# Kernel optimization log

Measured on AMD Instinct MI355X. Metric: run time of the kernel, lower is better.

## Reference

```python
import jax, jax.numpy as jnp
import numpy as np

B, C, H, W = 4, 256, 48, 48
HEADS, DH = 8, 64
HID = HEADS * DH
EPS = 1e-5
SCALE = DH ** -0.5


def setup_inputs() -> dict:
    key = jax.random.key(0)
    ks = jax.random.split(key, 8)
    return {
        "tensor": jax.random.normal(ks[0], (B, C, H, W), jnp.float32),
        "norm_g": jnp.ones((C,), jnp.float32),                      # ChanLayerNorm gamma
        "w_qkv": jax.random.normal(ks[1], (3 * HID, C), jnp.float32) * 0.02,  # 1x1 conv, no bias
        "dw_q": jax.random.normal(ks[2], (HID, 1, 3, 3), jnp.float32) * 0.1,  # depthwise 3x3
        "dw_k": jax.random.normal(ks[3], (HID, 1, 3, 3), jnp.float32) * 0.1,
        "dw_v": jax.random.normal(ks[4], (HID, 1, 3, 3), jnp.float32) * 0.1,
        "w_out": jax.random.normal(ks[5], (C, HID), jnp.float32) * 0.02,      # 1x1 conv out
        "b_out": jnp.zeros((C,), jnp.float32),
    }


def _rope(t):
    # t: (b, h, s, d) -- rotary embedding over flattened spatial positions
    s, d = t.shape[-2], t.shape[-1]
    inv_freq = 1.0 / (10000.0 ** (jnp.arange(0, d, 2, dtype=jnp.float32) / d))
    freqs = jnp.arange(s, dtype=jnp.float32)[:, None] * inv_freq[None, :]     # (s, d/2)
    emb = jnp.concatenate([freqs, freqs], axis=-1)                            # (s, d)
    cos, sin = jnp.cos(emb), jnp.sin(emb)
    t1, t2 = t[..., : d // 2], t[..., d // 2 :]
    rot = jnp.concatenate([-t2, t1], axis=-1)
    return t * cos + rot * sin


def _dwconv(x, w):
    # depthwise 3x3, padding=1 (Primer conv), groups = channels
    return jax.lax.conv_general_dilated(
        x, w, window_strides=(1, 1), padding="SAME",
        feature_group_count=x.shape[1],
        dimension_numbers=("NCHW", "OIHW", "NCHW"))


def reference(tensor, norm_g, w_qkv, dw_q, dw_k, dw_v, w_out, b_out):
    x = tensor
    # ChanLayerNorm: normalize over channel dim
    mean = jnp.mean(x, axis=1, keepdims=True)
    var = jnp.var(x, axis=1, keepdims=True)
    xn = (x - mean) * jax.lax.rsqrt(var + EPS) * norm_g[None, :, None, None]
    # 1x1 conv to qkv
    qkv = jnp.einsum("bchw,oc->bohw", xn, w_qkv)
    q, k, v = jnp.split(qkv, 3, axis=1)
    q, k, v = _dwconv(q, dw_q), _dwconv(k, dw_k), _dwconv(v, dw_v)
    # b (h d) x y -> b h (x y) d
    def to_seq(t):
        b = t.shape[0]
        return t.reshape(b, HEADS, DH, H * W).transpose(0, 1, 3, 2)
    q, k, v = to_seq(q), to_seq(k), to_seq(v)
    q, k = _rope(q), _rope(k)
    q = q * SCALE
    sim = jnp.einsum("bhid,bhjd->bhij", q, k)
    attn = jax.nn.softmax(sim, axis=-1)
    out = jnp.einsum("bhij,bhjd->bhid", attn, v)
    # b h (x y) d -> b (h d) x y
    out = out.transpose(0, 1, 3, 2).reshape(out.shape[0], HID, H, W)
    return jnp.einsum("bchw,oc->bohw", out, w_out) + b_out[None, :, None, None]
```

## Files before the change

### kernel.cpp

```cpp
#include <hip/hip_runtime.h>
#include <math.h>

#define SS 2304
#define C_IN 256
#define HID 512
#define QKV3 1536
#define HEADS 8
#define DH 64
#define BATCH 4
#define EPSV 1e-5f
#define SCALEV 0.125f

typedef short s8v __attribute__((ext_vector_type(8)));
typedef float f4v __attribute__((ext_vector_type(4)));
typedef unsigned int u4v __attribute__((ext_vector_type(4)));
typedef unsigned int uint32;

static __device__ inline unsigned short f2bf(float x) {
    unsigned int u = __float_as_uint(x);
    u += 0x7fffu + ((u >> 16) & 1u);
    return (unsigned short)(u >> 16);
}
static __device__ inline float bf2f(unsigned short h) {
    return __uint_as_float((unsigned int)h << 16);
}
static __device__ inline f4v mm(s8v a, s8v b, f4v c) {
    return __builtin_amdgcn_mfma_f32_16x16x32_bf16(a, b, c, 0, 0, 0);
}
static __device__ inline s8v pk4(uint32 a, uint32 b, uint32 c, uint32 d) {
    u4v t; t[0] = a; t[1] = b; t[2] = c; t[3] = d;
    return __builtin_bit_cast(s8v, t);
}
static __device__ inline uint32 pkhl(float p) {
    unsigned int u = __float_as_uint(p);
    unsigned int uh = u + (0x7fffu + ((u >> 16) & 1u));
    unsigned short h = (unsigned short)(uh >> 16);
    float r = p - __uint_as_float((unsigned int)h << 16);
    unsigned short l = (unsigned short)(__float_as_uint(r) >> 16);
    return (uint32)h | ((uint32)l << 16);
}
static __device__ inline uint32 rot16(uint32 u) { return (u >> 16) | (u << 16); }

__global__ void prep_wg(const float* __restrict__ w, const float* __restrict__ g,
                        float* __restrict__ wg, float* __restrict__ wsum) {
    __shared__ float red[256];
    int o = blockIdx.x, c = threadIdx.x;
    float v = w[o * C_IN + c] * g[c];
    wg[o * C_IN + c] = v;
    red[c] = v;
    __syncthreads();
    for (int st = 128; st > 0; st >>= 1) {
        if (c < st) red[c] += red[c + st];
        __syncthreads();
    }
    if (c == 0) wsum[o] = red[0];
}

__global__ void prep_rope(float* __restrict__ cosT, float* __restrict__ sinT) {
    int idx = blockIdx.x * 256 + threadIdx.x;
    if (idx >= SS * 32) return;
    int s = idx >> 5, f = idx & 31;
    double inv = pow(10000.0, -(double)f / 32.0);
    double ang = (double)s * inv;
    cosT[idx] = (float)cos(ang);
    sinT[idx] = (float)sin(ang);
}

__global__ void prep_stats(const float* __restrict__ x, float* __restrict__ mean,
                           float* __restrict__ rstd) {
    int p = blockIdx.x * 256 + threadIdx.x;
    int b = p / SS, s = p % SS;
    const float* xp = x + (size_t)b * C_IN * SS + s;
    float sm = 0.f;
    for (int c = 0; c < C_IN; ++c) sm += xp[(size_t)c * SS];
    float mu = sm * (1.0f / C_IN);
    float vs = 0.f;
    for (int c = 0; c < C_IN; ++c) { float d = xp[(size_t)c * SS] - mu; vs += d * d; }
    mean[p] = mu;
    rstd[p] = rsqrtf(vs * (1.0f / C_IN) + EPSV);
}

__global__ __launch_bounds__(256) void qkv_gemm(
    const float* __restrict__ x, const float* __restrict__ wg,
    const float* __restrict__ wsum, const float* __restrict__ mean,
    const float* __restrict__ rstd, float* __restrict__ qkv) {
    __shared__ float As[16][132];
    __shared__ float Bs[16][132];
    int b = blockIdx.z;
    int m0 = blockIdx.y * 128;
    int n0 = blockIdx.x * 128;
    int t = threadIdx.x;
    int tx = t & 15, ty = t >> 4;
    float acc[8][8] = {};
    const float* xb = x + (size_t)b * C_IN * SS;
    for (int k0 = 0; k0 < C_IN; k0 += 16) {
#pragma unroll
        for (int i = 0; i < 8; ++i) {
            int idx = t + i * 256;
            int kk = idx & 15, row = idx >> 4;
            As[kk][row] = wg[(m0 + row) * C_IN + k0 + kk];
            int ssi = idx & 127, cc = idx >> 7;
            Bs[cc][ssi] = xb[(size_t)(k0 + cc) * SS + n0 + ssi];
        }
        __syncthreads();
#pragma unroll
        for (int kk = 0; kk < 16; ++kk) {
            float4 a0 = *(const float4*)&As[kk][ty * 8];
            float4 a1 = *(const float4*)&As[kk][ty * 8 + 4];
            float4 b0 = *(const float4*)&Bs[kk][tx * 8];
            float4 b1 = *(const float4*)&Bs[kk][tx * 8 + 4];
            float am[8] = {a0.x, a0.y, a0.z, a0.w, a1.x, a1.y, a1.z, a1.w};
            float bn[8] = {b0.x, b0.y, b0.z, b0.w, b1.x, b1.y, b1.z, b1.w};
#pragma unroll
            for (int r = 0; r < 8; ++r)
#pragma unroll
                for (int c = 0; c < 8; ++c) acc[r][c] += am[r] * bn[c];
        }
        __syncthreads();
    }
    float mnv[8], rsv[8];
#pragma unroll
    for (int c = 0; c < 8; ++c) {
        int n = n0 + tx * 8 + c;
        mnv[c] = mean[b * SS + n];
        rsv[c] = rstd[b * SS + n];
    }
#pragma unroll
    for (int r = 0; r < 8; ++r) {
        int m = m0 + ty * 8 + r;
        float ws = wsum[m];
        float* dst = qkv + ((size_t)b * QKV3 + m) * SS + n0 + tx * 8;
        float ov[8];
#pragma unroll
        for (int c = 0; c < 8; ++c) ov[c] = rsv[c] * (acc[r][c] - mnv[c] * ws);
        *(float4*)dst = make_float4(ov[0], ov[1], ov[2], ov[3]);
        *(float4*)(dst + 4) = make_float4(ov[4], ov[5], ov[6], ov[7]);
    }
}

__global__ __launch_bounds__(256) void conv_rope(
    const float* __restrict__ qkv, const float* __restrict__ dwq,
    const float* __restrict__ dwk, const float* __restrict__ dwv,
    const float* __restrict__ cosT, const float* __restrict__ sinT,
    unsigned short* __restrict__ qhi, unsigned short* __restrict__ qlo,
    unsigned short* __restrict__ khi, unsigned short* __restrict__ klo,
    uint32* __restrict__ vtint) {
    __shared__ float tile[64][65];
    int b = blockIdx.z;
    int part = blockIdx.y >> 3;
    int h = blockIdx.y & 7;
    int s0 = blockIdx.x * 64;
    int t = threadIdx.x;
    int sl = t & 63, dgrp = t >> 6;
    int s = s0 + sl;
    int y = s / 48, xx = s - y * 48;
    int bh = b * HEADS + h;
    const float* dw = (part == 0) ? dwq : (part == 1) ? dwk : dwv;
#pragma unroll
    for (int i = 0; i < 16; ++i) {
        int d = dgrp * 16 + i;
        int cch = part * HID + h * DH + d;
        const float* src = qkv + ((size_t)b * QKV3 + cch) * SS;
        const float* wp = dw + (h * DH + d) * 9;
        float acc = 0.f;
#pragma unroll
        for (int dy = -1; dy <= 1; ++dy) {
            int yy = y + dy;
            if (yy < 0 || yy >= 48) continue;
#pragma unroll
            for (int dx = -1; dx <= 1; ++dx) {
                int xv = xx + dx;
                if (xv < 0 || xv >= 48) continue;
                acc += wp[(dy + 1) * 3 + (dx + 1)] * src[yy * 48 + xv];
            }
        }
        if (part == 2) {
            size_t o = ((size_t)bh * DH + d) * SS + s;
            unsigned short hu = f2bf(acc);
            unsigned short lu = (unsigned short)(__float_as_uint(acc - bf2f(hu)) >> 16);
            vtint[o] = (uint32)hu | ((uint32)lu << 16);
        } else {
            tile[d][sl] = acc;
        }
    }
    if (part == 2) return;
    __syncthreads();
    int d2 = t & 63, srow = t >> 6;
    unsigned short* hiA = (part == 0) ? qhi : khi;
    unsigned short* loA = (part == 0) ? qlo : klo;
#pragma unroll
    for (int i = 0; i < 16; ++i) {
        int sp = srow + 4 * i;
        float v0 = tile[d2][sp];
        float vp = tile[d2 ^ 32][sp];
        int f = d2 & 31;
        float cv = cosT[(s0 + sp) * 32 + f];
        float sv = sinT[(s0 + sp) * 32 + f];
        float rot = (d2 < 32) ? -vp : vp;
        float val = v0 * cv + rot * sv;
        if (part == 0) val *= SCALEV;
        size_t o = ((size_t)bh * SS + s0 + sp) * DH + d2;
        unsigned short hu = f2bf(val);
        hiA[o] = hu;
        loA[o] = f2bf(val - bf2f(hu));
    }
}

__global__ __launch_bounds__(256, 2) void attn_mfma(
    const unsigned short* __restrict__ qhi, const unsigned short* __restrict__ qlo,
    const unsigned short* __restrict__ khi, const unsigned short* __restrict__ klo,
    const uint32* __restrict__ vtint,
    float* __restrict__ Opart, float* __restrict__ lpart) {
    __shared__ float lds[4][64][68];
    __shared__ float lsl[4][64];
    int bh = blockIdx.z;
    int jh = blockIdx.y;
    int i0 = blockIdx.x * 64;
    int t = threadIdx.x;
    int wv = t >> 6;
    int lane = t & 63;
    int l15 = lane & 15;
    int quad = lane >> 4;

    s8v qf[4][4];
#pragma unroll
    for (int ig = 0; ig < 4; ++ig) {
        size_t qb = ((size_t)bh * SS + i0 + ig * 16 + l15) * DH + quad * 8;
        qf[ig][0] = *(const s8v*)(qhi + qb);
        qf[ig][1] = *(const s8v*)(qhi + qb + 32);
        qf[ig][2] = *(const s8v*)(qlo + qb);
        qf[ig][3] = *(const s8v*)(qlo + qb + 32);
    }
    f4v oacc[4][4];
#pragma unroll
    for (int dt = 0; dt < 4; ++dt)
#pragma unroll
        for (int ig = 0; ig < 4; ++ig) oacc[dt][ig] = (f4v){0.f, 0.f, 0.f, 0.f};
    float lsum[4] = {0.f, 0.f, 0.f, 0.f};

    const size_t kbh = (size_t)bh * SS * DH;
    const uint32* vbase = vtint + (size_t)bh * DH * SS;
    const int jbase = jh * 1152 + wv * 16;

    s8v kc[2][4], vc[2][4];
    auto ldK = [&](int s, s8v* K) {
        size_t row = kbh + (size_t)(jbase + s * 64 + l15) * DH + quad * 8;
        K[0] = *(const s8v*)(khi + row);
        K[1] = *(const s8v*)(khi + row + 32);
        K[2] = *(const s8v*)(klo + row);
        K[3] = *(const s8v*)(klo + row + 32);
    };
    auto ldV = [&](int s, s8v* V) {
        size_t col = (size_t)(jbase + s * 64 + quad * 4);
#pragma unroll
        for (int dt = 0; dt < 4; ++dt)
            V[dt] = __builtin_bit_cast(
                s8v, *(const u4v*)(vbase + (size_t)(dt * 16 + l15) * SS + col));
    };
    ldK(0, kc[0]);
    ldV(0, vc[0]);
#pragma unroll 2
    for (int s = 0; s < 18; ++s) {
        int cur = s & 1, nxt = cur ^ 1;
        if (s + 1 < 18) { ldK(s + 1, kc[nxt]); ldV(s + 1, vc[nxt]); }
        f4v sv[4];
#pragma unroll
        for (int ig = 0; ig < 4; ++ig) {
            f4v sx = {0.f, 0.f, 0.f, 0.f};
            sx = mm(kc[cur][0], qf[ig][0], sx);
            sx = mm(kc[cur][1], qf[ig][1], sx);
            sx = mm(kc[cur][0], qf[ig][2], sx);
            sx = mm(kc[cur][1], qf[ig][3], sx);
            sx = mm(kc[cur][2], qf[ig][0], sx);
            sx = mm(kc[cur][3], qf[ig][1], sx);
            sv[ig] = sx;
        }
        s8v B1[4], B2[4];
#pragma unroll
        for (int ig = 0; ig < 4; ++ig) {
            float p0 = __expf(sv[ig][0]), p1 = __expf(sv[ig][1]);
            float p2 = __expf(sv[ig][2]), p3 = __expf(sv[ig][3]);
            lsum[ig] += (p0 + p1) + (p2 + p3);
            uint32 u0 = pkhl(p0), u1 = pkhl(p1), u2 = pkhl(p2), u3 = pkhl(p3);
            B1[ig] = pk4(u0, u1, u2, u3);
            B2[ig] = pk4(rot16(u0), rot16(u1), rot16(u2), rot16(u3));
        }
#pragma unroll
        for (int dt = 0; dt < 4; ++dt)
#pragma unroll
            for (int ig = 0; ig < 4; ++ig) {
                oacc[dt][ig] = mm(vc[cur][dt], B1[ig], oacc[dt][ig]);
                oacc[dt][ig] = mm(vc[cur][dt], B2[ig], oacc[dt][ig]);
            }
    }
#pragma unroll
    for (int ig = 0; ig < 4; ++ig) {
        float v = lsum[ig];
        v += __shfl_xor(v, 16);
        v += __shfl_xor(v, 32);
        if (quad == 0) lsl[wv][ig * 16 + l15] = v;
    }
#pragma unroll
    for (int dt = 0; dt < 4; ++dt)
#pragma unroll
        for (int ig = 0; ig < 4; ++ig)
#pragma unroll
            for (int r = 0; r < 4; ++r)
                lds[wv][dt * 16 + quad * 4 + r][ig * 16 + l15] = oacc[dt][ig][r];
    __syncthreads();
    int d = t >> 2, qg = (t & 3) * 16;
    size_t ob = (((size_t)jh * 32 + bh) * DH + d) * SS + i0 + qg;
#pragma unroll
    for (int j4 = 0; j4 < 4; ++j4) {
        float4 a0 = *(const float4*)&lds[0][d][qg + j4 * 4];
        float4 a1 = *(const float4*)&lds[1][d][qg + j4 * 4];
        float4 a2 = *(const float4*)&lds[2][d][qg + j4 * 4];
        float4 a3 = *(const float4*)&lds[3][d][qg + j4 * 4];
        float4 rr;
        rr.x = (a0.x + a1.x) + (a2.x + a3.x);
        rr.y = (a0.y + a1.y) + (a2.y + a3.y);
        rr.z = (a0.z + a1.z) + (a2.z + a3.z);
        rr.w = (a0.w + a1.w) + (a2.w + a3.w);
        *(float4*)(Opart + ob + j4 * 4) = rr;
    }
    if (t < 64) {
        float v = (lsl[0][t] + lsl[1][t]) + (lsl[2][t] + lsl[3][t]);
        lpart[((size_t)jh * 32 + bh) * SS + i0 + t] = v;
    }
}

__global__ __launch_bounds__(256) void combine(
    const float* __restrict__ Opart, const float* __restrict__ lpart,
    float* __restrict__ OT) {
    int g = blockIdx.x * 256 + threadIdx.x;
    int s4 = g % (SS / 4);
    int rest = g / (SS / 4);
    int bh = rest >> 6;
    size_t base = (size_t)rest * SS + s4 * 4;
    float4 o0 = *(const float4*)(Opart + base);
    float4 o1 = *(const float4*)(Opart + base + (size_t)32 * DH * SS);
    float4 l0 = *(const float4*)(lpart + (size_t)bh * SS + s4 * 4);
    float4 l1 = *(const float4*)(lpart + (size_t)(32 + bh) * SS + s4 * 4);
    float4 r;
    r.x = (o0.x + o1.x) / (l0.x + l1.x);
    r.y = (o0.y + o1.y) / (l0.y + l1.y);
    r.z = (o0.z + o1.z) / (l0.z + l1.z);
    r.w = (o0.w + o1.w) / (l0.w + l1.w);
    *(float4*)(OT + base) = r;
}

__global__ __launch_bounds__(256) void outproj(
    const float* __restrict__ OT, const float* __restrict__ w_out,
    const float* __restrict__ b_out, float* __restrict__ out) {
    __shared__ float As[16][68];
    __shared__ float Bs[16][132];
    int b = blockIdx.z;
    int m0 = blockIdx.y * 64;
    int n0 = blockIdx.x * 128;
    int t = threadIdx.x;
    int tx = t & 15, ty = t >> 4;
    float acc[4][8] = {};
    for (int k0 = 0; k0 < HID; k0 += 16) {
        const float* OTb = OT + ((size_t)b * HID + k0) * SS + n0;
#pragma unroll
        for (int i = 0; i < 4; ++i) {
            int idx = t + i * 256;
            int kk = idx & 15, mm2 = idx >> 4;
            As[kk][mm2] = w_out[(m0 + mm2) * HID + k0 + kk];
        }
#pragma unroll
        for (int i = 0; i < 8; ++i) {
            int idx = t + i * 256;
            int kk = idx >> 7, nn = idx & 127;
            Bs[kk][nn] = OTb[(size_t)kk * SS + nn];
        }
        __syncthreads();
#pragma unroll
        for (int kk = 0; kk < 16; ++kk) {
            float4 av = *(const float4*)&As[kk][ty * 4];
            float4 b0 = *(const float4*)&Bs[kk][tx * 8];
            float4 b1 = *(const float4*)&Bs[kk][tx * 8 + 4];
            float aa[4] = {av.x, av.y, av.z, av.w};
            float bb[8] = {b0.x, b0.y, b0.z, b0.w, b1.x, b1.y, b1.z, b1.w};
#pragma unroll
            for (int r = 0; r < 4; ++r)
#pragma unroll
                for (int c = 0; c < 8; ++c) acc[r][c] += aa[r] * bb[c];
        }
        __syncthreads();
    }
#pragma unroll
    for (int r = 0; r < 4; ++r) {
        int o = m0 + ty * 4 + r;
        float bo = b_out[o];
        float* dst = out + ((size_t)b * C_IN + o) * SS + n0 + tx * 8;
        float ov[8];
#pragma unroll
        for (int c = 0; c < 8; ++c) ov[c] = acc[r][c] + bo;
        *(float4*)dst = make_float4(ov[0], ov[1], ov[2], ov[3]);
        *(float4*)(dst + 4) = make_float4(ov[4], ov[5], ov[6], ov[7]);
    }
}

extern "C" void kernel_launch(void* const* d_in, const int* in_sizes, int n_in,
                              void* d_out, int out_size, void* d_ws, size_t ws_size,
                              hipStream_t stream) {
    (void)in_sizes; (void)n_in; (void)out_size; (void)ws_size;
    const float* x     = (const float*)d_in[0];
    const float* g     = (const float*)d_in[1];
    const float* w_qkv = (const float*)d_in[2];
    const float* dwq   = (const float*)d_in[3];
    const float* dwk   = (const float*)d_in[4];
    const float* dwv   = (const float*)d_in[5];
    const float* w_out = (const float*)d_in[6];
    const float* b_out = (const float*)d_in[7];
    float* out = (float*)d_out;

    char* ws = (char*)d_ws;
    size_t off = 0;
    auto alloc = [&](size_t nbytes) -> void* {
        char* p = ws + off;
        off = (off + nbytes + 255) & ~(size_t)255;
        return (void*)p;
    };
    const size_t NSD = (size_t)BATCH * HEADS * SS * DH;
    float* wg   = (float*)alloc((size_t)QKV3 * C_IN * 4);
    float* wsum = (float*)alloc((size_t)QKV3 * 4);
    float* mean = (float*)alloc((size_t)BATCH * SS * 4);
    float* rstd = (float*)alloc((size_t)BATCH * SS * 4);
    float* cosT = (float*)alloc((size_t)SS * 32 * 4);
    float* sinT = (float*)alloc((size_t)SS * 32 * 4);
    float* qkv  = (float*)alloc((size_t)BATCH * QKV3 * SS * 4);
    unsigned short* qhi  = (unsigned short*)alloc(NSD * 2);
    unsigned short* qlo  = (unsigned short*)alloc(NSD * 2);
    unsigned short* khi  = (unsigned short*)alloc(NSD * 2);
    unsigned short* klo  = (unsigned short*)alloc(NSD * 2);
    uint32* vtint = (uint32*)alloc(NSD * 4);
    float* lpart = (float*)alloc((size_t)2 * 32 * SS * 4);
    float* Opart = qkv;
    float* OT    = qkv + 2 * NSD;

    prep_wg<<<QKV3, 256, 0, stream>>>(w_qkv, g, wg, wsum);
    prep_rope<<<288, 256, 0, stream>>>(cosT, sinT);
    prep_stats<<<36, 256, 0, stream>>>(x, mean, rstd);
    qkv_gemm<<<dim3(18, 12, BATCH), 256, 0, stream>>>(x, wg, wsum, mean, rstd, qkv);
    conv_rope<<<dim3(36, 24, BATCH), 256, 0, stream>>>(qkv, dwq, dwk, dwv, cosT, sinT,
                                                       qhi, qlo, khi, klo, vtint);
    attn_mfma<<<dim3(36, 2, 32), 256, 0, stream>>>(qhi, qlo, khi, klo, vtint,
                                                   Opart, lpart);
    combine<<<4608, 256, 0, stream>>>(Opart, lpart, OT);
    outproj<<<dim3(18, 4, BATCH), 256, 0, stream>>>(OT, w_out, b_out, out);
}
```

Measured before the change: 526.9 us.

## Move QKV and output projections to split-bf16 MFMA with transposed packed operands

Replaces the FP32 SIMT GEMMs for the QKV projection and the output projection with bf16 MFMA kernels. Each operand is packed as hi/lo bf16 pairs, giving a three-term split product for near-FP32 accuracy. Adds an x transpose/pack kernel and a weight-packing kernel, and folds the head-combine step into a transposing pack, so both GEMMs read K-contiguous operands straight from global memory into registers. The attention probabilities now use a truncating hi/lo split instead of a rounding one, which is slightly cheaper. The cost is extra pack passes and uncoalesced scalar epilogue stores.

```diff
diff --git a/kernel.cpp b/kernel.cpp
--- a/kernel.cpp
+++ b/kernel.cpp
@@ -31,22 +31,30 @@
     u4v t; t[0] = a; t[1] = b; t[2] = c; t[3] = d;
     return __builtin_bit_cast(s8v, t);
 }
-static __device__ inline uint32 pkhl(float p) {
-    unsigned int u = __float_as_uint(p);
-    unsigned int uh = u + (0x7fffu + ((u >> 16) & 1u));
-    unsigned short h = (unsigned short)(uh >> 16);
-    float r = p - __uint_as_float((unsigned int)h << 16);
-    unsigned short l = (unsigned short)(__float_as_uint(r) >> 16);
-    return (uint32)h | ((uint32)l << 16);
+static __device__ inline uint32 pk_rnd(float x) {
+    unsigned int u = __float_as_uint(x);
+    unsigned int uh = (u + (0x7fffu + ((u >> 16) & 1u))) & 0xffff0000u;
+    float r = x - __uint_as_float(uh);
+    return (uh >> 16) | (__float_as_uint(r) & 0xffff0000u);
+}
+static __device__ inline uint32 pk_trunc(float x) {
+    unsigned int u = __float_as_uint(x);
+    unsigned int h = u & 0xffff0000u;
+    float r = x - __uint_as_float(h);
+    return (h >> 16) | (__float_as_uint(r) & 0xffff0000u);
 }
 static __device__ inline uint32 rot16(uint32 u) { return (u >> 16) | (u << 16); }
-
-__global__ void prep_wg(const float* __restrict__ w, const float* __restrict__ g,
-                        float* __restrict__ wg, float* __restrict__ wsum) {
+static __device__ inline u4v rot16v(u4v u) {
+    u4v r; r[0] = rot16(u[0]); r[1] = rot16(u[1]); r[2] = rot16(u[2]); r[3] = rot16(u[3]);
+    return r;
+}
+
+__global__ void prep_wgint(const float* __restrict__ w, const float* __restrict__ g,
+                           uint32* __restrict__ wgint, float* __restrict__ wsum) {
     __shared__ float red[256];
     int o = blockIdx.x, c = threadIdx.x;
     float v = w[o * C_IN + c] * g[c];
-    wg[o * C_IN + c] = v;
+    wgint[o * C_IN + c] = pk_rnd(v);
     red[c] = v;
     __syncthreads();
     for (int st = 128; st > 0; st >>= 1) {
@@ -54,6 +62,11 @@
         __syncthreads();
     }
     if (c == 0) wsum[o] = red[0];
+}
+
+__global__ void prep_woutint(const float* __restrict__ w, uint32* __restrict__ wi) {
+    int idx = blockIdx.x * 256 + threadIdx.x;
+    wi[idx] = pk_rnd(w[idx]);
 }
 
 __global__ void prep_rope(float* __restrict__ cosT, float* __restrict__ sinT) {
@@ -80,62 +93,93 @@
     rstd[p] = rsqrtf(vs * (1.0f / C_IN) + EPSV);
 }
 
-__global__ __launch_bounds__(256) void qkv_gemm(
-    const float* __restrict__ x, const float* __restrict__ wg,
+__global__ __launch_bounds__(256) void xt_pack(const float* __restrict__ x,
+                                               uint32* __restrict__ xTint) {
+    __shared__ float tile[64][65];
+    int b = blockIdx.z;
+    int c0 = blockIdx.y * 64;
+    int s0 = blockIdx.x * 64;
+    int t = threadIdx.x;
+    int sl = t & 63, cg = t >> 6;
+#pragma unroll
+    for (int i = 0; i < 16; ++i) {
+        int c = cg * 16 + i;
+        tile[c][sl] = x[((size_t)b * C_IN + c0 + c) * SS + s0 + sl];
+    }
+    __syncthreads();
+    int cl = t & 63, sg = t >> 6;
+#pragma unroll
+    for (int i = 0; i < 16; ++i) {
+        int s = sg * 16 + i;
+        xTint[((size_t)b * SS + s0 + s) * C_IN + c0 + cl] = pk_rnd(tile[cl][s]);
+    }
+}
+
+__global__ __launch_bounds__(256, 4) void qkv_mfma(
+    const uint32* __restrict__ wgint, const uint32* __restrict__ xTint,
     const float* __restrict__ wsum, const float* __restrict__ mean,
     const float* __restrict__ rstd, float* __restrict__ qkv) {
-    __shared__ float As[16][132];
-    __shared__ float Bs[16][132];
     int b = blockIdx.z;
     int m0 = blockIdx.y * 128;
-    int n0 = blockIdx.x * 128;
+    int n0 = blockIdx.x * 64;
     int t = threadIdx.x;
-    int tx = t & 15, ty = t >> 4;
-    float acc[8][8] = {};
-    const float* xb = x + (size_t)b * C_IN * SS;
-    for (int k0 = 0; k0 < C_IN; k0 += 16) {
-#pragma unroll
-        for (int i = 0; i < 8; ++i) {
-            int idx = t + i * 256;
-            int kk = idx & 15, row = idx >> 4;
-            As[kk][row] = wg[(m0 + row) * C_IN + k0 + kk];
-            int ssi = idx & 127, cc = idx >> 7;
-            Bs[cc][ssi] = xb[(size_t)(k0 + cc) * SS + n0 + ssi];
-        }
-        __syncthreads();
-#pragma unroll
-        for (int kk = 0; kk < 16; ++kk) {
-            float4 a0 = *(const float4*)&As[kk][ty * 8];
-            float4 a1 = *(const float4*)&As[kk][ty * 8 + 4];
-            float4 b0 = *(const float4*)&Bs[kk][tx * 8];
-            float4 b1 = *(const float4*)&Bs[kk][tx * 8 + 4];
-            float am[8] = {a0.x, a0.y, a0.z, a0.w, a1.x, a1.y, a1.z, a1.w};
-            float bn[8] = {b0.x, b0.y, b0.z, b0.w, b1.x, b1.y, b1.z, b1.w};
-#pragma unroll
-            for (int r = 0; r < 8; ++r)
-#pragma unroll
-                for (int c = 0; c < 8; ++c) acc[r][c] += am[r] * bn[c];
-        }
-        __syncthreads();
-    }
-    float mnv[8], rsv[8];
-#pragma unroll
-    for (int c = 0; c < 8; ++c) {
-        int n = n0 + tx * 8 + c;
-        mnv[c] = mean[b * SS + n];
-        rsv[c] = rstd[b * SS + n];
-    }
-#pragma unroll
-    for (int r = 0; r < 8; ++r) {
-        int m = m0 + ty * 8 + r;
-        float ws = wsum[m];
-        float* dst = qkv + ((size_t)b * QKV3 + m) * SS + n0 + tx * 8;
-        float ov[8];
-#pragma unroll
-        for (int c = 0; c < 8; ++c) ov[c] = rsv[c] * (acc[r][c] - mnv[c] * ws);
-        *(float4*)dst = make_float4(ov[0], ov[1], ov[2], ov[3]);
-        *(float4*)(dst + 4) = make_float4(ov[4], ov[5], ov[6], ov[7]);
-    }
+    int wv = t >> 6, lane = t & 63, l15 = lane & 15, quad = lane >> 4;
+    int wm = wv * 32;
+    const uint32* Ab = wgint + (size_t)(m0 + wm) * C_IN;
+    const uint32* Bb = xTint + ((size_t)b * SS + n0) * C_IN;
+    f4v acc[2][4];
+#pragma unroll
+    for (int mt = 0; mt < 2; ++mt)
+#pragma unroll
+        for (int nt = 0; nt < 4; ++nt) acc[mt][nt] = (f4v){0.f, 0.f, 0.f, 0.f};
+    u4v af[2][2], bf[2][4];
+    auto ldA = [&](int ch, u4v* A) {
+#pragma unroll
+        for (int mt = 0; mt < 2; ++mt)
+            A[mt] = *(const u4v*)(Ab + (size_t)(mt * 16 + l15) * C_IN + ch * 16 + quad * 4);
+    };
+    auto ldB = [&](int ch, u4v* B) {
+#pragma unroll
+        for (int nt = 0; nt < 4; ++nt)
+            B[nt] = *(const u4v*)(Bb + (size_t)(nt * 16 + l15) * C_IN + ch * 16 + quad * 4);
+    };
+    ldA(0, af[0]);
+    ldB(0, bf[0]);
+#pragma unroll 2
+    for (int ch = 0; ch < 16; ++ch) {
+        int cur = ch & 1, nxt = cur ^ 1;
+        if (ch + 1 < 16) { ldA(ch + 1, af[nxt]); ldB(ch + 1, bf[nxt]); }
+        u4v br[4];
+#pragma unroll
+        for (int nt = 0; nt < 4; ++nt) br[nt] = rot16v(bf[cur][nt]);
+#pragma unroll
+        for (int mt = 0; mt < 2; ++mt) {
+            s8v a = __builtin_bit_cast(s8v, af[cur][mt]);
+#pragma unroll
+            for (int nt = 0; nt < 4; ++nt) {
+                acc[mt][nt] = mm(a, __builtin_bit_cast(s8v, bf[cur][nt]), acc[mt][nt]);
+                acc[mt][nt] = mm(a, __builtin_bit_cast(s8v, br[nt]), acc[mt][nt]);
+            }
+        }
+    }
+    float mnv[4], rsv[4];
+#pragma unroll
+    for (int nt = 0; nt < 4; ++nt) {
+        int n = n0 + nt * 16 + l15;
+        mnv[nt] = mean[b * SS + n];
+        rsv[nt] = rstd[b * SS + n];
+    }
+#pragma unroll
+    for (int mt = 0; mt < 2; ++mt)
+#pragma unroll
+        for (int r = 0; r < 4; ++r) {
+            int m = m0 + wm + mt * 16 + quad * 4 + r;
+            float ws = wsum[m];
+            float* dst = qkv + ((size_t)b * QKV3 + m) * SS + n0 + l15;
+#pragma unroll
+            for (int nt = 0; nt < 4; ++nt)
+                dst[nt * 16] = rsv[nt] * (acc[mt][nt][r] - mnv[nt] * ws);
+        }
 }
 
 __global__ __launch_bounds__(256) void conv_rope(
@@ -176,9 +220,7 @@
         }
         if (part == 2) {
             size_t o = ((size_t)bh * DH + d) * SS + s;
-            unsigned short hu = f2bf(acc);
-            unsigned short lu = (unsigned short)(__float_as_uint(acc - bf2f(hu)) >> 16);
-            vtint[o] = (uint32)hu | ((uint32)lu << 16);
+            vtint[o] = pk_rnd(acc);
         } else {
             tile[d][sl] = acc;
         }
@@ -281,7 +323,8 @@
             float p0 = __expf(sv[ig][0]), p1 = __expf(sv[ig][1]);
             float p2 = __expf(sv[ig][2]), p3 = __expf(sv[ig][3]);
             lsum[ig] += (p0 + p1) + (p2 + p3);
-            uint32 u0 = pkhl(p0), u1 = pkhl(p1), u2 = pkhl(p2), u3 = pkhl(p3);
+            uint32 u0 = pk_trunc(p0), u1 = pk_trunc(p1);
+            uint32 u2 = pk_trunc(p2), u3 = pk_trunc(p3);
             B1[ig] = pk4(u0, u1, u2, u3);
             B2[ig] = pk4(rot16(u0), rot16(u1), rot16(u2), rot16(u3));
         }
@@ -329,77 +372,89 @@
     }
 }
 
-__global__ __launch_bounds__(256) void combine(
+__global__ __launch_bounds__(256) void combine_t(
     const float* __restrict__ Opart, const float* __restrict__ lpart,
-    float* __restrict__ OT) {
-    int g = blockIdx.x * 256 + threadIdx.x;
-    int s4 = g % (SS / 4);
-    int rest = g / (SS / 4);
-    int bh = rest >> 6;
-    size_t base = (size_t)rest * SS + s4 * 4;
-    float4 o0 = *(const float4*)(Opart + base);
-    float4 o1 = *(const float4*)(Opart + base + (size_t)32 * DH * SS);
-    float4 l0 = *(const float4*)(lpart + (size_t)bh * SS + s4 * 4);
-    float4 l1 = *(const float4*)(lpart + (size_t)(32 + bh) * SS + s4 * 4);
-    float4 r;
-    r.x = (o0.x + o1.x) / (l0.x + l1.x);
-    r.y = (o0.y + o1.y) / (l0.y + l1.y);
-    r.z = (o0.z + o1.z) / (l0.z + l1.z);
-    r.w = (o0.w + o1.w) / (l0.w + l1.w);
-    *(float4*)(OT + base) = r;
-}
-
-__global__ __launch_bounds__(256) void outproj(
-    const float* __restrict__ OT, const float* __restrict__ w_out,
+    uint32* __restrict__ OTint) {
+    __shared__ uint32 tile[64][65];
+    int bh = blockIdx.y;
+    int s0 = blockIdx.x * 64;
+    int b = bh >> 3, h = bh & 7;
+    int t = threadIdx.x;
+    int sl = t & 63, dg = t >> 6;
+    float linv = 1.f / (lpart[(size_t)bh * SS + s0 + sl] +
+                        lpart[(size_t)(32 + bh) * SS + s0 + sl]);
+#pragma unroll
+    for (int i = 0; i < 16; ++i) {
+        int d = dg * 16 + i;
+        size_t off = ((size_t)bh * DH + d) * SS + s0 + sl;
+        float v = (Opart[off] + Opart[off + (size_t)32 * DH * SS]) * linv;
+        tile[d][sl] = pk_rnd(v);
+    }
+    __syncthreads();
+    int dl = t & 63, sg = t >> 6;
+#pragma unroll
+    for (int i = 0; i < 16; ++i) {
+        int s = sg * 16 + i;
+        OTint[((size_t)b * SS + s0 + s) * HID + h * DH + dl] = tile[dl][s];
+    }
+}
+
+__global__ __launch_bounds__(256, 4) void outproj_mfma(
+    const uint32* __restrict__ OTint, const uint32* __restrict__ woutint,
     const float* __restrict__ b_out, float* __restrict__ out) {
-    __shared__ float As[16][68];
-    __shared__ float Bs[16][132];
     int b = blockIdx.z;
-    int m0 = blockIdx.y * 64;
+    int m0 = blockIdx.y * 32;
     int n0 = blockIdx.x * 128;
     int t = threadIdx.x;
-    int tx = t & 15, ty = t >> 4;
-    float acc[4][8] = {};
-    for (int k0 = 0; k0 < HID; k0 += 16) {
-        const float* OTb = OT + ((size_t)b * HID + k0) * SS + n0;
-#pragma unroll
-        for (int i = 0; i < 4; ++i) {
-            int idx = t + i * 256;
-            int kk = idx & 15, mm2 = idx >> 4;
-            As[kk][mm2] = w_out[(m0 + mm2) * HID + k0 + kk];
-        }
-#pragma unroll
-        for (int i = 0; i < 8; ++i) {
-            int idx = t + i * 256;
-            int kk = idx >> 7, nn = idx & 127;
-            Bs[kk][nn] = OTb[(size_t)kk * SS + nn];
-        }
-        __syncthreads();
-#pragma unroll
-        for (int kk = 0; kk < 16; ++kk) {
-            float4 av = *(const float4*)&As[kk][ty * 4];
-            float4 b0 = *(const float4*)&Bs[kk][tx * 8];
-            float4 b1 = *(const float4*)&Bs[kk][tx * 8 + 4];
-            float aa[4] = {av.x, av.y, av.z, av.w};
-            float bb[8] = {b0.x, b0.y, b0.z, b0.w, b1.x, b1.y, b1.z, b1.w};
-#pragma unroll
-            for (int r = 0; r < 4; ++r)
-#pragma unroll
-                for (int c = 0; c < 8; ++c) acc[r][c] += aa[r] * bb[c];
-        }
-        __syncthreads();
-    }
-#pragma unroll
-    for (int r = 0; r < 4; ++r) {
-        int o = m0 + ty * 4 + r;
-        float bo = b_out[o];
-        float* dst = out + ((size_t)b * C_IN + o) * SS + n0 + tx * 8;
-        float ov[8];
-#pragma unroll
-        for (int c = 0; c < 8; ++c) ov[c] = acc[r][c] + bo;
-        *(float4*)dst = make_float4(ov[0], ov[1], ov[2], ov[3]);
-        *(float4*)(dst + 4) = make_float4(ov[4], ov[5], ov[6], ov[7]);
-    }
+    int wv = t >> 6, lane = t & 63, l15 = lane & 15, quad = lane >> 4;
+    int wn = wv * 32;
+    const uint32* Ab = woutint + (size_t)m0 * HID;
+    const uint32* Bb = OTint + ((size_t)b * SS + n0 + wn) * HID;
+    f4v acc[2][2];
+#pragma unroll
+    for (int mt = 0; mt < 2; ++mt)
+#pragma unroll
+        for (int nt = 0; nt < 2; ++nt) acc[mt][nt] = (f4v){0.f, 0.f, 0.f, 0.f};
+    u4v af[2][2], bf[2][2];
+    auto ldA = [&](int ch, u4v* A) {
+#pragma unroll
+        for (int mt = 0; mt < 2; ++mt)
+            A[mt] = *(const u4v*)(Ab + (size_t)(mt * 16 + l15) * HID + ch * 16 + quad * 4);
+    };
+    auto ldB = [&](int ch, u4v* B) {
+#pragma unroll
+        for (int nt = 0; nt < 2; ++nt)
+            B[nt] = *(const u4v*)(Bb + (size_t)(nt * 16 + l15) * HID + ch * 16 + quad * 4);
+    };
+    ldA(0, af[0]);
+    ldB(0, bf[0]);
+#pragma unroll 2
+    for (int ch = 0; ch < 32; ++ch) {
+        int cur = ch & 1, nxt = cur ^ 1;
+        if (ch + 1 < 32) { ldA(ch + 1, af[nxt]); ldB(ch + 1, bf[nxt]); }
+        u4v br[2];
+#pragma unroll
+        for (int nt = 0; nt < 2; ++nt) br[nt] = rot16v(bf[cur][nt]);
+#pragma unroll
+        for (int mt = 0; mt < 2; ++mt) {
+            s8v a = __builtin_bit_cast(s8v, af[cur][mt]);
+#pragma unroll
+            for (int nt = 0; nt < 2; ++nt) {
+                acc[mt][nt] = mm(a, __builtin_bit_cast(s8v, bf[cur][nt]), acc[mt][nt]);
+                acc[mt][nt] = mm(a, __builtin_bit_cast(s8v, br[nt]), acc[mt][nt]);
+            }
+        }
+    }
+#pragma unroll
+    for (int mt = 0; mt < 2; ++mt)
+#pragma unroll
+        for (int r = 0; r < 4; ++r) {
+            int o = m0 + mt * 16 + quad * 4 + r;
+            float bo = b_out[o];
+            float* dst = out + ((size_t)b * C_IN + o) * SS + n0 + wn + l15;
+#pragma unroll
+            for (int nt = 0; nt < 2; ++nt) dst[nt * 16] = acc[mt][nt][r] + bo;
+        }
 }
 
 extern "C" void kernel_launch(void* const* d_in, const int* in_sizes, int n_in,
@@ -424,7 +479,8 @@
         return (void*)p;
     };
     const size_t NSD = (size_t)BATCH * HEADS * SS * DH;
-    float* wg   = (float*)alloc((size_t)QKV3 * C_IN * 4);
+    uint32* wgint   = (uint32*)alloc((size_t)QKV3 * C_IN * 4);
+    uint32* woutint = (uint32*)alloc((size_t)C_IN * HID * 4);
     float* wsum = (float*)alloc((size_t)QKV3 * 4);
     float* mean = (float*)alloc((size_t)BATCH * SS * 4);
     float* rstd = (float*)alloc((size_t)BATCH * SS * 4);
@@ -437,17 +493,20 @@
     unsigned short* klo  = (unsigned short*)alloc(NSD * 2);
     uint32* vtint = (uint32*)alloc(NSD * 4);
     float* lpart = (float*)alloc((size_t)2 * 32 * SS * 4);
-    float* Opart = qkv;
-    float* OT    = qkv + 2 * NSD;
-
-    prep_wg<<<QKV3, 256, 0, stream>>>(w_qkv, g, wg, wsum);
+    uint32* xTint = (uint32*)qhi;
+    float*  Opart = qkv;
+    uint32* OTint = (uint32*)(qkv + 2 * NSD);
+
+    prep_wgint<<<QKV3, 256, 0, stream>>>(w_qkv, g, wgint, wsum);
+    prep_woutint<<<512, 256, 0, stream>>>(w_out, woutint);
     prep_rope<<<288, 256, 0, stream>>>(cosT, sinT);
     prep_stats<<<36, 256, 0, stream>>>(x, mean, rstd);
-    qkv_gemm<<<dim3(18, 12, BATCH), 256, 0, stream>>>(x, wg, wsum, mean, rstd, qkv);
+    xt_pack<<<dim3(36, 4, BATCH), 256, 0, stream>>>(x, xTint);
+    qkv_mfma<<<dim3(36, 12, BATCH), 256, 0, stream>>>(wgint, xTint, wsum, mean, rstd, qkv);
     conv_rope<<<dim3(36, 24, BATCH), 256, 0, stream>>>(qkv, dwq, dwk, dwv, cosT, sinT,
                                                        qhi, qlo, khi, klo, vtint);
     attn_mfma<<<dim3(36, 2, 32), 256, 0, stream>>>(qhi, qlo, khi, klo, vtint,
                                                    Opart, lpart);
-    combine<<<4608, 256, 0, stream>>>(Opart, lpart, OT);
-    outproj<<<dim3(18, 4, BATCH), 256, 0, stream>>>(OT, w_out, b_out, out);
-}
+    combine_t<<<dim3(36, 32), 256, 0, stream>>>(Opart, lpart, OTint);
+    outproj_mfma<<<dim3(18, 8, BATCH), 256, 0, stream>>>(OTint, woutint, b_out, out);
+}
```

New measurement: 497.0 us. -5.7%, faster.
